# Kernel optimization log

Hardware: AMD Instinct MI355X
Metric: run time of the kernel (lower is better)

The kernel has to match this reference:

```python
import jax, jax.numpy as jnp
import numpy as np

N = 50000   # num_node
E = 1600000 # edge_size (N * avg_degree 32)
B = 64      # batch, hardcoded via repeat(64,1,1) in the torch module


def setup_inputs() -> dict:
    key = jax.random.key(0)
    k = jax.random.split(key, 8)
    return {
        "t": jax.random.normal(k[0], (1,), dtype=jnp.float32),
        "input": jax.random.normal(k[1], (B, N), dtype=jnp.float32),
        "edge_i": jax.random.randint(k[2], (E,), 0, N, dtype=jnp.int32),
        "edge_j": jax.random.randint(k[3], (E,), 0, N, dtype=jnp.int32),
        "weight_react": jax.random.normal(k[4], (1, E), dtype=jnp.float32) / 10.0,
        "weight_diff": jax.random.normal(k[5], (1, E), dtype=jnp.float32) / 1000.0,
        "bias_reaction": jax.random.normal(k[6], (1, N), dtype=jnp.float32) / 10.0,
        "bias_diffusion": jax.random.normal(k[7], (1, N), dtype=jnp.float32) / 10.0,
    }


def _lap_matvec(x, w, src, dst, n):
    # W[src_e, dst_e] = w_e (duplicates coalesce by sum, as torch sparse_coo_tensor does)
    # L = diag(colsum(W)) - W ; returns x @ L^T applied batched: out[b, v] = (L x[b])[v]
    col = jax.ops.segment_sum(w, dst, num_segments=n)                 # [N] column sums
    msg = jax.ops.segment_sum(w[:, None] * x[:, dst].T, src,
                              num_segments=n)                          # [N, B]
    return col[None, :] * x - msg.T                                   # [B, N]


def reference(t, input, edge_i, edge_j, weight_react, weight_diff,
              bias_reaction, bias_diffusion):
    x = input                                                          # [B, N]
    n = x.shape[1]
    # reaction Laplacian uses edges (i -> j); diffusion uses transposed (j -> i)
    reaction = _lap_matvec(x, weight_react[0], edge_i, edge_j, n) + bias_reaction
    diffusion = _lap_matvec(x, weight_diff[0], edge_j, edge_i, n) + bias_diffusion
    # up and down both True: tanh(reaction) + diffusion + input
    return jnp.tanh(reaction) + diffusion + x
```

## Files before the change

### kernel.cpp

```cpp
#include <hip/hip_runtime.h>
#include <hip/hip_fp16.h>


#define BKT_SHIFT 7
#define BKT_NODES 128
#define RCAP 4608
#define RCAP2 5504
#define CH 4096
#define NBP 512

#define RFL(x) __builtin_amdgcn_readfirstlane(x)

__device__ __forceinline__ unsigned bf16_rne(float f) {
    unsigned u = __float_as_uint(f);
    unsigned rb = (u >> 16) & 1u;
    u += 0x7FFFu + rb;
    return u >> 16;
}
__device__ __forceinline__ float bf16_lo(int y) {
    return __uint_as_float(((unsigned)y) << 16);
}
__device__ __forceinline__ float bf16_hi(int y) {
    return __uint_as_float((unsigned)y & 0xFFFF0000u);
}

__global__ void transpose_kernel(const float* __restrict__ x, __half* __restrict__ xth,
                                 int* __restrict__ gcur, int ngcur, int N) {
    __shared__ float tile[64][65];
    int v0 = blockIdx.x * 64;
    int tx = threadIdx.x;
    int ty = threadIdx.y;
    int flat = blockIdx.x * 1024 + ty * 64 + tx;
    if (flat < ngcur) gcur[flat] = 0;
    if (v0 + tx < N) {
        for (int b = ty; b < 64; b += 16)
            tile[tx][b] = x[b * N + v0 + tx];
    }
    __syncthreads();
    for (int vl = ty; vl < 64; vl += 16) {
        int v = v0 + vl;
        if (v < N)
            xth[(size_t)v * 64 + tx] = __float2half(tile[vl][tx]);
    }
}

__global__ void __launch_bounds__(512) partition_kernel(
        const int* __restrict__ ei, const int* __restrict__ ej,
        const float* __restrict__ wr, const float* __restrict__ wd,
        int* __restrict__ gcur, int2* __restrict__ runs,
        int E, int NB) {
    __shared__ int cnt[2 * NBP];
    __shared__ int base_a[2 * NBP];
    __shared__ int gb[2 * NBP];
    __shared__ int2 buf[2 * CH];

    int tid = threadIdx.x;
    int e0 = blockIdx.x * CH;
    int ch_len = min(CH, E - e0);
    if (ch_len <= 0) return;

    int my_i[8], my_j[8];
    unsigned my_w[8];
    #pragma unroll
    for (int k = 0; k < 8; ++k) {
        int t = tid + k * 512;
        if (t < ch_len) {
            int e = e0 + t;
            my_i[k] = ei[e];
            my_j[k] = ej[e];
            my_w[k] = (bf16_rne(wr[e]) << 16) | bf16_rne(wd[e]);
        } else {
            my_i[k] = -1;
        }
    }

    for (int b = tid; b < 2 * NBP; b += 512) cnt[b] = 0;
    __syncthreads();
    #pragma unroll
    for (int k = 0; k < 8; ++k) {
        if (my_i[k] >= 0) {
            atomicAdd(&cnt[my_i[k] >> BKT_SHIFT], 1);
            atomicAdd(&cnt[NBP + (my_j[k] >> BKT_SHIFT)], 1);
        }
    }
    __syncthreads();
    if (tid < 64) {
        int carry = 0;
        #pragma unroll
        for (int c = 0; c < (2 * NBP) / 64; ++c) {
            int idx = c * 64 + tid;
            int val = cnt[idx];
            int scan = val;
            for (int off = 1; off < 64; off <<= 1) {
                int n = __shfl_up(scan, off, 64);
                if (tid >= off) scan += n;
            }
            int excl = scan - val + carry;
            base_a[idx] = excl;
            cnt[idx] = excl;
            carry += __shfl(scan, 63, 64);
        }
    }
    __syncthreads();
    #pragma unroll
    for (int k = 0; k < 8; ++k) {
        if (my_i[k] >= 0) {
            int i = my_i[k], j = my_j[k];
            unsigned wv = my_w[k];
            int b0 = i >> BKT_SHIFT;
            int p0 = atomicAdd(&cnt[b0], 1);
            buf[p0] = make_int2((int)(((unsigned)b0 << 23) | ((unsigned)(i & 127) << 16) | (unsigned)j),
                                (int)wv);
            int b1 = j >> BKT_SHIFT;
            int p1 = atomicAdd(&cnt[NBP + b1], 1);
            buf[p1] = make_int2((int)(((unsigned)b1 << 23) | ((unsigned)(j & 127) << 16) | (unsigned)i),
                                (int)((wv << 16) | (wv >> 16)));
        }
    }
    __syncthreads();
    for (int cb = tid; cb < 2 * NBP; cb += 512) {
        int n = cnt[cb] - base_a[cb];
        if (n > 0) {
            int side = cb >> 9;
            int bkt = cb & (NBP - 1);
            gb[cb] = atomicAdd(&gcur[side * NB + bkt], n);
        }
    }
    __syncthreads();
    int total = 2 * ch_len;
    for (int t = tid; t < total; t += 512) {
        int2 p = buf[t];
        int side = (t >= ch_len) ? 1 : 0;
        int bkt = ((unsigned)p.x >> 23) & 0x1FF;
        int cb = side * NBP + bkt;
        int rank = gb[cb] + (t - base_a[cb]);
        if (rank < RCAP)
            runs[((size_t)(side * NB + bkt)) * RCAP + rank] = p;
    }
}

#define ACC4(P, D)                                                        \
    {                                                                     \
        float wv_ = bf16_hi(P);                                           \
        float2 f_;                                                        \
        f_ = __half22float2(*(const __half2*)&(D).x);                     \
        a0 = fmaf(wv_, f_.x, a0); a1 = fmaf(wv_, f_.y, a1);               \
        f_ = __half22float2(*(const __half2*)&(D).y);                     \
        a2 = fmaf(wv_, f_.x, a2); a3 = fmaf(wv_, f_.y, a3);               \
    }

#define COMB3(A) { A += __shfl_xor(A, 8); A += __shfl_xor(A, 16); A += __shfl_xor(A, 32); }

__global__ void __launch_bounds__(512) sortgather_kernel(
        const int* __restrict__ gcur, const int2* __restrict__ runs,
        const __half* __restrict__ xth,
        __half* __restrict__ msg, float* __restrict__ colsum,
        int NB, int N, int h) {
    __shared__ int cnt[BKT_NODES];
    __shared__ int cur[BKT_NODES];
    __shared__ int pb[BKT_NODES];
    __shared__ float csum[BKT_NODES];
    __shared__ int dst[RCAP2];

    int sb = blockIdx.x;
    int side = (sb >= NB) ? 1 : 0;
    int b = sb - side * NB;
    int v0 = b << BKT_SHIFT;
    int len = min(gcur[sb], RCAP);
    size_t roff = (size_t)sb * RCAP;
    int tid = threadIdx.x;

    int2 my[9];
    #pragma unroll
    for (int k = 0; k < 9; ++k) {
        int t = tid + k * 512;
        if (t < len) my[k] = runs[roff + t];
        else my[k].x = -1;
    }

    if (tid < BKT_NODES) { cnt[tid] = 0; csum[tid] = 0.f; }
    __syncthreads();
    #pragma unroll
    for (int k = 0; k < 9; ++k) {
        if (my[k].x != -1) {
            int dl = ((unsigned)my[k].x >> 16) & 0x7F;
            atomicAdd(&cnt[dl], 1);
            if (h == 0) atomicAdd(&csum[dl], bf16_lo(my[k].y));
        }
    }
    __syncthreads();
    if (tid < 64) {
        int carry = 0;
        #pragma unroll
        for (int c = 0; c < BKT_NODES / 64; ++c) {
            int idx = c * 64 + tid;
            int val = (cnt[idx] + 7) & ~7;
            int scan = val;
            for (int off = 1; off < 64; off <<= 1) {
                int n = __shfl_up(scan, off, 64);
                if (tid >= off) scan += n;
            }
            int excl = scan - val + carry;
            pb[idx] = excl;
            cur[idx] = excl;
            carry += __shfl(scan, 63, 64);
        }
    }
    __syncthreads();
    if (tid < BKT_NODES) {
        int pc = (cnt[tid] + 7) & ~7;
        for (int t = cnt[tid]; t < pc; ++t) dst[pb[tid] + t] = 0;
    }
    __syncthreads();
    #pragma unroll
    for (int k = 0; k < 9; ++k) {
        if (my[k].x != -1) {
            int dl = ((unsigned)my[k].x >> 16) & 0x7F;
            int pos = atomicAdd(&cur[dl], 1);
            dst[pos] = (int)(((unsigned)my[k].y & 0xFFFF0000u) | ((unsigned)my[k].x & 0xFFFFu));
        }
    }
    __syncthreads();

    const uint2* __restrict__ xq = (const uint2*)xth;
    int lane = tid & 63;
    int g  = lane >> 3;
    int bl = lane & 7;
    int hb = h * 8 + (lane & 7);
    int wid = tid >> 6;
    for (int t = 0; t < BKT_NODES / 8; ++t) {
        int dl = wid * (BKT_NODES / 8) + t;
        int v = v0 + dl;
        if (v >= N) continue;
        const int* pay = dst + pb[dl] + g;
        int noct = ((cnt[dl] + 7) & ~7) >> 3;
        float a0 = 0.f, a1 = 0.f, a2 = 0.f, a3 = 0.f;
        int o = 0;
        for (; o + 4 <= noct; o += 4) {
            int pA = pay[8 * o];
            int pB = pay[8 * o + 8];
            int pC = pay[8 * o + 16];
            int pD = pay[8 * o + 24];
            uint2 dA = xq[(((size_t)((unsigned)pA & 0xFFFFu)) << 4) + hb];
            uint2 dB = xq[(((size_t)((unsigned)pB & 0xFFFFu)) << 4) + hb];
            uint2 dC = xq[(((size_t)((unsigned)pC & 0xFFFFu)) << 4) + hb];
            uint2 dD = xq[(((size_t)((unsigned)pD & 0xFFFFu)) << 4) + hb];
            ACC4(pA, dA)
            ACC4(pB, dB)
            ACC4(pC, dC)
            ACC4(pD, dD)
        }
        for (; o < noct; ++o) {
            int p = pay[8 * o];
            uint2 d = xq[(((size_t)((unsigned)p & 0xFFFFu)) << 4) + hb];
            ACC4(p, d)
        }
        COMB3(a0) COMB3(a1) COMB3(a2) COMB3(a3)
        if (lane < 8) {
            __half2 h0 = __floats2half2_rn(a0, a1);
            __half2 h1 = __floats2half2_rn(a2, a3);
            uint2 st = make_uint2(*(unsigned*)&h0, *(unsigned*)&h1);
            *(uint2*)(msg + ((size_t)side * N + v) * 64 + h * 32 + 4 * lane) = st;
        }
        if (h == 0 && lane == 0)
            colsum[(size_t)side * N + v] = csum[dl];
    }
}

__global__ void final_kernel(const float* __restrict__ x,
                             const __half* __restrict__ msg,
                             const float* __restrict__ colsum,
                             const float* __restrict__ br, const float* __restrict__ bd,
                             float* __restrict__ out, int N) {
    __shared__ float tr[64][65];
    __shared__ float td[64][65];
    int v0 = blockIdx.x * 64;
    int tx = threadIdx.x;
    int ty = threadIdx.y;
    for (int vl = ty; vl < 64; vl += 16) {
        int v = v0 + vl;
        if (v < N) {
            tr[vl][tx] = __half2float(msg[(size_t)v * 64 + tx]);
            td[vl][tx] = __half2float(msg[((size_t)N + v) * 64 + tx]);
        }
    }
    __syncthreads();
    int v = v0 + tx;
    if (v < N) {
        float cold = colsum[v];
        float colr = colsum[(size_t)N + v];
        float brv = br[v], bdv = bd[v];
        for (int b = ty; b < 64; b += 16) {
            float xv = x[b * N + v];
            float r = colr * xv - tr[tx][b] + brv;
            float d = cold * xv - td[tx][b] + bdv;
            out[b * N + v] = tanhf(r) + d + xv;
        }
    }
}

extern "C" void kernel_launch(void* const* d_in, const int* in_sizes, int n_in,
                              void* d_out, int out_size, void* d_ws, size_t ws_size,
                              hipStream_t stream) {
    const float* x  = (const float*)d_in[1];
    const int*   ei = (const int*)d_in[2];
    const int*   ej = (const int*)d_in[3];
    const float* wr = (const float*)d_in[4];
    const float* wd = (const float*)d_in[5];
    const float* br = (const float*)d_in[6];
    const float* bd = (const float*)d_in[7];
    float* out = (float*)d_out;

    int E = in_sizes[2];
    int N = in_sizes[6];
    int NB = (N + BKT_NODES - 1) >> BKT_SHIFT;
    (void)out_size; (void)ws_size; (void)n_in;

    char* w = (char*)d_ws;
    __half* xth = (__half*)w;    w += (size_t)N * 64 * 2;
    __half* msg = (__half*)w;    w += (size_t)2 * N * 64 * 2;
    float* colsum = (float*)w;   w += (size_t)2 * N * 4;
    int* gcur   = (int*)w;       w += (size_t)2 * NB * 4;
    w = (char*)(((uintptr_t)w + 15) & ~(uintptr_t)15);
    int2* runs  = (int2*)w;

    dim3 tb(64, 16);
    int ntiles = (N + 63) / 64;
    transpose_kernel<<<ntiles, tb, 0, stream>>>(x, xth, gcur, 2 * NB, N);

    int nchunks = (E + CH - 1) / CH;
    partition_kernel<<<nchunks, 512, 0, stream>>>(ei, ej, wr, wd, gcur, runs, E, NB);

    sortgather_kernel<<<2 * NB, 512, 0, stream>>>(gcur, runs, xth, msg, colsum, NB, N, 0);
    sortgather_kernel<<<2 * NB, 512, 0, stream>>>(gcur, runs, xth, msg, colsum, NB, N, 1);

    final_kernel<<<ntiles, tb, 0, stream>>>(x, msg, colsum, br, bd, out, N);
}
```

Measured before the change: 227.3 us.

## Split half-precision x into batch-half planes and reuse sorted runs across gather passes

The transposed half-precision x is now stored as two separate 32-wide batch planes, so each gather pass reads a compact plane that is half the size and can stay in cache better. The first pass sorts edges by destination as before, then writes the sorted payload plus the per-node offsets and counts back into the runs buffer in place. A new second kernel loads that pre-sorted list directly, so it no longer repeats the counting sort and the atomics. Both passes also switch to nontemporal loads and stores for the streaming data. The in-place overwrite of runs depends on each block reading only its own region before writing it, and on the RCAP*2 stride being large enough to hold the offset and count arrays.

```diff
diff --git a/kernel.cpp b/kernel.cpp
--- a/kernel.cpp
+++ b/kernel.cpp
@@ -8,8 +8,9 @@
 #define RCAP2 5504
 #define CH 4096
 #define NBP 512
-
-#define RFL(x) __builtin_amdgcn_readfirstlane(x)
+#define RSTRIDE (RCAP * 2)
+#define PB_OFF 8192
+#define CNT_OFF 8320
 
 __device__ __forceinline__ unsigned bf16_rne(float f) {
     unsigned u = __float_as_uint(f);
@@ -37,10 +38,12 @@
             tile[tx][b] = x[b * N + v0 + tx];
     }
     __syncthreads();
+    size_t plane = (size_t)(tx >> 5) * N * 32;
+    int bl = tx & 31;
     for (int vl = ty; vl < 64; vl += 16) {
         int v = v0 + vl;
         if (v < N)
-            xth[(size_t)v * 64 + tx] = __float2half(tile[vl][tx]);
+            xth[plane + (size_t)v * 32 + bl] = __float2half(tile[vl][tx]);
     }
 }
 
@@ -151,11 +154,61 @@
 
 #define COMB3(A) { A += __shfl_xor(A, 8); A += __shfl_xor(A, 16); A += __shfl_xor(A, 32); }
 
+__device__ __forceinline__ void gather_plane(
+        const int* cnt, const int* pb, const int* dst,
+        const __half* __restrict__ plane, __half* __restrict__ msg,
+        const float* csum, float* colsum,
+        int side, int v0, int N, int half, int tid) {
+    const uint2* __restrict__ xq = (const uint2*)plane;
+    int lane = tid & 63;
+    int g  = lane >> 3;
+    int bl = lane & 7;
+    int wid = tid >> 6;
+    for (int t = 0; t < BKT_NODES / 8; ++t) {
+        int dl = wid * (BKT_NODES / 8) + t;
+        int v = v0 + dl;
+        if (v >= N) continue;
+        const int* pay = dst + pb[dl] + g;
+        int noct = ((cnt[dl] + 7) & ~7) >> 3;
+        float a0 = 0.f, a1 = 0.f, a2 = 0.f, a3 = 0.f;
+        int o = 0;
+        for (; o + 4 <= noct; o += 4) {
+            int pA = pay[8 * o];
+            int pB = pay[8 * o + 8];
+            int pC = pay[8 * o + 16];
+            int pD = pay[8 * o + 24];
+            uint2 dA = xq[(((size_t)((unsigned)pA & 0xFFFFu)) << 3) + bl];
+            uint2 dB = xq[(((size_t)((unsigned)pB & 0xFFFFu)) << 3) + bl];
+            uint2 dC = xq[(((size_t)((unsigned)pC & 0xFFFFu)) << 3) + bl];
+            uint2 dD = xq[(((size_t)((unsigned)pD & 0xFFFFu)) << 3) + bl];
+            ACC4(pA, dA)
+            ACC4(pB, dB)
+            ACC4(pC, dC)
+            ACC4(pD, dD)
+        }
+        for (; o < noct; ++o) {
+            int p = pay[8 * o];
+            uint2 d = xq[(((size_t)((unsigned)p & 0xFFFFu)) << 3) + bl];
+            ACC4(p, d)
+        }
+        COMB3(a0) COMB3(a1) COMB3(a2) COMB3(a3)
+        if (lane < 8) {
+            __half2 h0 = __floats2half2_rn(a0, a1);
+            __half2 h1 = __floats2half2_rn(a2, a3);
+            uint2 st = make_uint2(*(unsigned*)&h0, *(unsigned*)&h1);
+            __builtin_nontemporal_store(*(long long*)&st,
+                (long long*)(msg + ((size_t)side * N + v) * 64 + half * 32 + 4 * lane));
+        }
+        if (colsum && lane == 0)
+            colsum[(size_t)side * N + v] = csum[dl];
+    }
+}
+
 __global__ void __launch_bounds__(512) sortgather_kernel(
-        const int* __restrict__ gcur, const int2* __restrict__ runs,
+        const int* __restrict__ gcur, const int2* runs, int* dstg,
         const __half* __restrict__ xth,
         __half* __restrict__ msg, float* __restrict__ colsum,
-        int NB, int N, int h) {
+        int NB, int N) {
     __shared__ int cnt[BKT_NODES];
     __shared__ int cur[BKT_NODES];
     __shared__ int pb[BKT_NODES];
@@ -174,8 +227,11 @@
     #pragma unroll
     for (int k = 0; k < 9; ++k) {
         int t = tid + k * 512;
-        if (t < len) my[k] = runs[roff + t];
-        else my[k].x = -1;
+        if (t < len) {
+            long long raw = __builtin_nontemporal_load((const long long*)(runs + roff + t));
+            my[k].x = (int)(unsigned)(raw & 0xFFFFFFFFll);
+            my[k].y = (int)(unsigned)((unsigned long long)raw >> 32);
+        } else my[k].x = -1;
     }
 
     if (tid < BKT_NODES) { cnt[tid] = 0; csum[tid] = 0.f; }
@@ -185,7 +241,7 @@
         if (my[k].x != -1) {
             int dl = ((unsigned)my[k].x >> 16) & 0x7F;
             atomicAdd(&cnt[dl], 1);
-            if (h == 0) atomicAdd(&csum[dl], bf16_lo(my[k].y));
+            atomicAdd(&csum[dl], bf16_lo(my[k].y));
         }
     }
     __syncthreads();
@@ -222,49 +278,47 @@
     }
     __syncthreads();
 
-    const uint2* __restrict__ xq = (const uint2*)xth;
-    int lane = tid & 63;
-    int g  = lane >> 3;
-    int bl = lane & 7;
-    int hb = h * 8 + (lane & 7);
-    int wid = tid >> 6;
-    for (int t = 0; t < BKT_NODES / 8; ++t) {
-        int dl = wid * (BKT_NODES / 8) + t;
-        int v = v0 + dl;
-        if (v >= N) continue;
-        const int* pay = dst + pb[dl] + g;
-        int noct = ((cnt[dl] + 7) & ~7) >> 3;
-        float a0 = 0.f, a1 = 0.f, a2 = 0.f, a3 = 0.f;
-        int o = 0;
-        for (; o + 4 <= noct; o += 4) {
-            int pA = pay[8 * o];
-            int pB = pay[8 * o + 8];
-            int pC = pay[8 * o + 16];
-            int pD = pay[8 * o + 24];
-            uint2 dA = xq[(((size_t)((unsigned)pA & 0xFFFFu)) << 4) + hb];
-            uint2 dB = xq[(((size_t)((unsigned)pB & 0xFFFFu)) << 4) + hb];
-            uint2 dC = xq[(((size_t)((unsigned)pC & 0xFFFFu)) << 4) + hb];
-            uint2 dD = xq[(((size_t)((unsigned)pD & 0xFFFFu)) << 4) + hb];
-            ACC4(pA, dA)
-            ACC4(pB, dB)
-            ACC4(pC, dC)
-            ACC4(pD, dD)
-        }
-        for (; o < noct; ++o) {
-            int p = pay[8 * o];
-            uint2 d = xq[(((size_t)((unsigned)p & 0xFFFFu)) << 4) + hb];
-            ACC4(p, d)
-        }
-        COMB3(a0) COMB3(a1) COMB3(a2) COMB3(a3)
-        if (lane < 8) {
-            __half2 h0 = __floats2half2_rn(a0, a1);
-            __half2 h1 = __floats2half2_rn(a2, a3);
-            uint2 st = make_uint2(*(unsigned*)&h0, *(unsigned*)&h1);
-            *(uint2*)(msg + ((size_t)side * N + v) * 64 + h * 32 + 4 * lane) = st;
-        }
-        if (h == 0 && lane == 0)
-            colsum[(size_t)side * N + v] = csum[dl];
-    }
+    int tot = pb[BKT_NODES - 1] + ((cnt[BKT_NODES - 1] + 7) & ~7);
+    int* reg = dstg + (size_t)sb * RSTRIDE;
+    for (int t2 = tid; 2 * t2 < tot; t2 += 512) {
+        long long v8 = *(const long long*)&dst[2 * t2];
+        __builtin_nontemporal_store(v8, (long long*)reg + t2);
+    }
+    if (tid < BKT_NODES) {
+        reg[PB_OFF + tid] = pb[tid];
+        reg[CNT_OFF + tid] = cnt[tid];
+    }
+
+    gather_plane(cnt, pb, dst, xth, msg, csum, colsum, side, v0, N, 0, tid);
+}
+
+__global__ void __launch_bounds__(512) gather1_kernel(
+        const int* dstg, const __half* __restrict__ xth1,
+        __half* __restrict__ msg, int NB, int N) {
+    __shared__ int cnt[BKT_NODES];
+    __shared__ int pb[BKT_NODES];
+    __shared__ int dst[RCAP2];
+
+    int sb = blockIdx.x;
+    int side = (sb >= NB) ? 1 : 0;
+    int b = sb - side * NB;
+    int v0 = b << BKT_SHIFT;
+    int tid = threadIdx.x;
+    const int* reg = dstg + (size_t)sb * RSTRIDE;
+
+    if (tid < BKT_NODES) {
+        pb[tid] = reg[PB_OFF + tid];
+        cnt[tid] = reg[CNT_OFF + tid];
+    }
+    __syncthreads();
+    int tot = pb[BKT_NODES - 1] + ((cnt[BKT_NODES - 1] + 7) & ~7);
+    for (int t2 = tid; 2 * t2 < tot; t2 += 512) {
+        long long v8 = __builtin_nontemporal_load((const long long*)reg + t2);
+        *(long long*)&dst[2 * t2] = v8;
+    }
+    __syncthreads();
+
+    gather_plane(cnt, pb, dst, xth1, msg, nullptr, nullptr, side, v0, N, 1, tid);
 }
 
 __global__ void final_kernel(const float* __restrict__ x,
@@ -331,8 +385,10 @@
     int nchunks = (E + CH - 1) / CH;
     partition_kernel<<<nchunks, 512, 0, stream>>>(ei, ej, wr, wd, gcur, runs, E, NB);
 
-    sortgather_kernel<<<2 * NB, 512, 0, stream>>>(gcur, runs, xth, msg, colsum, NB, N, 0);
-    sortgather_kernel<<<2 * NB, 512, 0, stream>>>(gcur, runs, xth, msg, colsum, NB, N, 1);
+    sortgather_kernel<<<2 * NB, 512, 0, stream>>>(gcur, runs, (int*)runs, xth,
+                                                  msg, colsum, NB, N);
+    gather1_kernel<<<2 * NB, 512, 0, stream>>>((const int*)runs,
+                                               xth + (size_t)N * 32, msg, NB, N);
 
     final_kernel<<<ntiles, tb, 0, stream>>>(x, msg, colsum, br, bd, out, N);
 }
```

Result: no change. 228.3 us (+0.5%).
